# Kernel tuning notes

Hardware: AMD Instinct MI355X
Metric: run time of the kernel (lower is better)

The kernel has to match this reference:

```python
import jax, jax.numpy as jnp
import numpy as np
import math

B, T, C, NH, NLQ, NLKV, DHR = 2, 1024, 2048, 16, 512, 512, 64
HS = C // NH


def _rope(x, cos, sin):
    # x: [B,T,H,D]; cos/sin: [T,D//2]. Rotates pairs (even,odd) like torch apply_rotary_emb.
    xr = x.reshape(x.shape[:-1] + (-1, 2))
    re, im = xr[..., 0], xr[..., 1]
    c = cos[None, :, None, :]
    s = sin[None, :, None, :]
    out = jnp.stack([re * c - im * s, re * s + im * c], axis=-1)
    return out.reshape(x.shape)


def setup_inputs() -> dict:
    key = jax.random.key(0)
    ks = jax.random.split(key, 9)
    sc = jnp.float32(0.02)
    x = jax.random.normal(ks[0], (B, T, C), jnp.float32)
    W_dq = jax.random.normal(ks[1], (NLQ, C), jnp.float32) * sc
    W_uq = jax.random.normal(ks[2], (C, NLQ), jnp.float32) * sc
    W_dkv = jax.random.normal(ks[3], (NLKV, C), jnp.float32) * sc
    W_uk = jax.random.normal(ks[4], (C, NLKV), jnp.float32) * sc
    W_uv = jax.random.normal(ks[5], (C, NLKV), jnp.float32) * sc
    W_qr = jax.random.normal(ks[6], (NH * DHR, NLQ), jnp.float32) * sc
    W_kr = jax.random.normal(ks[7], (DHR, C), jnp.float32) * sc
    W_o = jax.random.normal(ks[8], (C, C), jnp.float32) * sc
    inv = 1.0 / (10000.0 ** (np.arange(0, DHR, 2, dtype=np.float64) / DHR))
    fr = np.outer(np.arange(T), inv)
    freqs_cos = jnp.asarray(np.cos(fr), jnp.float32)
    freqs_sin = jnp.asarray(np.sin(fr), jnp.float32)
    return {"x": x, "freqs_cos": freqs_cos, "freqs_sin": freqs_sin,
            "W_dq": W_dq, "W_uq": W_uq, "W_dkv": W_dkv, "W_uk": W_uk,
            "W_uv": W_uv, "W_qr": W_qr, "W_kr": W_kr, "W_o": W_o}


def reference(x, freqs_cos, freqs_sin, W_dq, W_uq, W_dkv, W_uk, W_uv, W_qr, W_kr, W_o):
    # Training path of FullMHLA (no kv_cache, dropout=0).
    # Absorbed matrices: same memory reinterpretation as torch .view on [out,in] weights.
    k_eff = jnp.einsum('qhd,hdk->hqk', W_uq.reshape(NLQ, NH, HS), W_uk.reshape(NH, HS, NLKV))  # [nh,nlq,nlkv]
    v_eff = (W_uv.T @ W_o.T).reshape(NLKV, NH, HS)  # used as [nlkv,nh,hs]

    c_q = x @ W_dq.T            # [B,T,nlq]
    c_kv = x @ W_dkv.T          # [B,T,nlkv]

    # content scores: c_q @ k_eff @ c_kv^T
    q_abs = jnp.einsum('btq,hqk->bhtk', c_q, k_eff)          # [B,nh,T,nlkv]
    attn_c = jnp.einsum('bhtk,bsk->bhts', q_abs, c_kv)       # [B,nh,T,T]

    # decoupled RoPE scores
    c_kr = x @ W_kr.T                                         # [B,T,dhr]
    k_r = _rope(c_kr[:, :, None, :], freqs_cos, freqs_sin)[:, :, 0, :]   # [B,T,dhr]
    c_qr = (c_q @ W_qr.T).reshape(B, T, NH, DHR)
    q_r = _rope(c_qr, freqs_cos, freqs_sin)                   # [B,T,nh,dhr]
    attn_r = jnp.einsum('bthd,bsd->bhts', q_r, k_r)           # [B,nh,T,T]

    attn = (attn_c + attn_r) / math.sqrt(HS + DHR)
    mask = jnp.triu(jnp.ones((T, T), dtype=bool), k=1)
    attn = jnp.where(mask[None, None], jnp.float32(-jnp.inf), attn)
    attn = jax.nn.softmax(attn, axis=-1)

    # y = attn @ c_kv @ v_eff
    lat = jnp.einsum('bhts,bsk->bhtk', attn, c_kv)            # [B,nh,T,nlkv]
    y = jnp.einsum('bhtk,khd->bthd', lat, v_eff)              # [B,T,nh,hs]
    return y.reshape(B, T, C)
```

## Files before the change

### kernel.cpp

```cpp
#include <hip/hip_runtime.h>

#define Bv   2
#define Tv   1024
#define Cv   2048
#define NHv  16

typedef unsigned short u16;
typedef __attribute__((ext_vector_type(8))) short bf8_t;
typedef __attribute__((ext_vector_type(4))) float f4_t;
typedef __attribute__((ext_vector_type(4))) unsigned short u16x4;
typedef __attribute__((ext_vector_type(8))) unsigned short u16x8;

__device__ __forceinline__ u16 f2bf(float f) {
  union { float f; unsigned u; } v; v.f = f;
  unsigned r = v.u + 0x7fffu + ((v.u >> 16) & 1u);
  return (u16)(r >> 16);
}
__device__ __forceinline__ float bf2f(u16 b) {
  return __uint_as_float((unsigned)b << 16);
}
__device__ __forceinline__ void glds16(const u16* gp, u16* lp) {
  __builtin_amdgcn_global_load_lds(
      (const __attribute__((address_space(1))) void*)gp,
      (__attribute__((address_space(3))) void*)lp, 16, 0, 0);
}

struct Job {
  const u16* A; const u16* B; void* C;
  long sA1, sA2, sB1, sB2, sC1, sC2;
  int K, lda, ldb, ldc, Nact, zdiv, ntx, nty, out_bf;
};
struct JobPack3 { Job j[3]; int cum[4]; };

__global__ __launch_bounds__(256) void gemm_multi(JobPack3 P) {
  const int bid = blockIdx.x;
  const int ji = (bid >= P.cum[1] ? 1 : 0) + (bid >= P.cum[2] ? 1 : 0);
  const Job& J = P.j[ji];
  int local = bid - P.cum[ji];
  const int x = local % J.ntx;
  int rest = local / J.ntx;
  const int y = rest % J.nty;
  const int z = rest / J.nty;
  const int m0 = y * 128, n0 = x * 128;

  const int z1 = z / J.zdiv, z2 = z % J.zdiv;
  const u16* A = J.A + z1 * J.sA1 + z2 * J.sA2;
  const u16* B = J.B + z1 * J.sB1 + z2 * J.sB2;
  const int K = J.K, lda = J.lda, ldb = J.ldb, ldc = J.ldc, Nact = J.Nact;

  __shared__ u16 SMEM[16384];
  u16* As = SMEM;
  u16* Bs = SMEM + 8192;

  const int tid = threadIdx.x, w = tid >> 6, ln = tid & 63;
  const int my = w >> 1, mx = w & 1;
  const int g = ln >> 4, m = ln & 15;

  f4_t acc[4][4];
#pragma unroll
  for (int i = 0; i < 4; ++i)
#pragma unroll
    for (int j = 0; j < 4; ++j) acc[i][j] = (f4_t)0.f;

  for (int k0 = 0; k0 < K; k0 += 64) {
#pragma unroll
    for (int q = 0; q < 4; ++q) {
      int r = 32 * w + 8 * q + (ln >> 3);
      int c = ((ln & 7) - r) & 7;
      glds16(&A[(long)(m0 + r) * lda + k0 + c * 8], &As[(32 * w + 8 * q) * 64]);
      glds16(&B[(long)(n0 + r) * ldb + k0 + c * 8], &Bs[(32 * w + 8 * q) * 64]);
    }
    __syncthreads();
#pragma unroll
    for (int kh = 0; kh < 2; ++kh) {
      bf8_t af[4], bg[4];
#pragma unroll
      for (int mt = 0; mt < 4; ++mt) {
        int row = my * 64 + mt * 16 + m;
        af[mt] = *(const bf8_t*)&As[row * 64 + (((kh * 4 + g) + row) & 7) * 8];
      }
#pragma unroll
      for (int nt = 0; nt < 4; ++nt) {
        int row = mx * 64 + nt * 16 + m;
        bg[nt] = *(const bf8_t*)&Bs[row * 64 + (((kh * 4 + g) + row) & 7) * 8];
      }
#pragma unroll
      for (int mt = 0; mt < 4; ++mt)
#pragma unroll
        for (int nt = 0; nt < 4; ++nt)
          acc[mt][nt] = __builtin_amdgcn_mfma_f32_16x16x32_bf16(
              af[mt], bg[nt], acc[mt][nt], 0, 0, 0);
    }
    __syncthreads();
  }

  if (J.out_bf) {
    u16* Es = SMEM + w * 4096;
#pragma unroll
    for (int mt = 0; mt < 4; ++mt)
#pragma unroll
      for (int nt = 0; nt < 4; ++nt)
#pragma unroll
        for (int r = 0; r < 4; ++r) {
          int row = mt * 16 + g * 4 + r;
          int col = nt * 16 + m;
          Es[row * 64 + (((col >> 3) + row) & 7) * 8 + (col & 7)] =
              f2bf(acc[mt][nt][r]);
        }
    __syncthreads();
    u16* C = (u16*)J.C + z1 * J.sC1 + z2 * J.sC2;
    const long rowbase = (long)(m0 + my * 64 + ln) * ldc + n0 + mx * 64;
#pragma unroll
    for (int c = 0; c < 8; ++c) {
      if (n0 + mx * 64 + c * 8 < Nact) {
        u16x8 v = *(const u16x8*)&Es[ln * 64 + ((c + ln) & 7) * 8];
        *(u16x8*)&C[rowbase + c * 8] = v;
      }
    }
  } else {
    float* C = (float*)J.C + z1 * J.sC1 + z2 * J.sC2;
#pragma unroll
    for (int mt = 0; mt < 4; ++mt)
#pragma unroll
      for (int nt = 0; nt < 4; ++nt)
#pragma unroll
        for (int r = 0; r < 4; ++r) {
          int row = m0 + my * 64 + mt * 16 + g * 4 + r;
          int col = n0 + mx * 64 + nt * 16 + m;
          if (col < Nact) C[(long)row * ldc + col] = acc[mt][nt][r];
        }
  }
}

__global__ __launch_bounds__(256, 3) void attn_part(
    const u16* __restrict__ Qcat,
    const u16* __restrict__ Kcat,
    const u16* __restrict__ ZT,
    float* __restrict__ Opart,
    float* __restrict__ ml,
    float* __restrict__ out) {
  const int x = blockIdx.x;
  const int bh = x & 31, item = x >> 5;
  const int b = bh >> 4, h = bh & 15;
  static const int qtab[40] = {2,3,4,5,6,6,7,7,8,8,9,9,10,10,10,11,11,11,
                               12,12,12,13,13,13,14,14,14,14,15,15,15,15,
                               0,1,4,5,8,9,12,13};
  static const int ctab[40] = {0,0,0,0,0,1,0,1,0,1,0,1,0,1,2,0,1,2,
                               0,1,2,0,1,2,0,1,2,3,0,1,2,3,
                               0,0,1,1,2,2,3,3};
  const int qt = qtab[item], ch = ctab[item];
  const int ns = (qt >> 1) + 1;
  const int s0t = 2 * ch, s1t = min(2 * ch + 2, ns);
  const bool full = (ch == 0) && (qt <= 3);

  __shared__ u16 Bs[8192];
  __shared__ u16 Ps[8192];

  const int tid = threadIdx.x, w = tid >> 6, ln = tid & 63;
  const int g = ln >> 4, m = ln & 15;

  const u16* Qb = Qcat + (long)bh * 589824 + (long)qt * 64 * 576;
  const u16* Kb = Kcat + (long)b * 589824;
  const u16* Zb = ZT + (long)bh * 131072;

  const long qoff = (long)(16 * w + m) * 576;

  f4_t O[8];
#pragma unroll
  for (int j = 0; j < 8; ++j) O[j] = (f4_t)0.f;
  float mrow[4], lrow[4];
#pragma unroll
  for (int r = 0; r < 4; ++r) { mrow[r] = -3e38f; lrow[r] = 0.f; }

  const float scale = 0.07216878364870322f;

  for (int st = s0t; st < s1t; ++st) {
    f4_t S[8];
#pragma unroll
    for (int j = 0; j < 8; ++j) S[j] = (f4_t)0.f;

#pragma unroll 1
    for (int k0 = 0; k0 < 576; k0 += 64) {
#pragma unroll
      for (int q = 0; q < 4; ++q) {
        int r = 32 * w + 8 * q + (ln >> 3);
        int c = ((ln & 7) - r) & 7;
        glds16(&Kb[(long)(st * 128 + r) * 576 + k0 + c * 8],
               &Bs[(32 * w + 8 * q) * 64]);
      }
      bf8_t af0 = *(const bf8_t*)&Qb[qoff + k0 + g * 8];
      bf8_t af1 = *(const bf8_t*)&Qb[qoff + k0 + 32 + g * 8];
      __syncthreads();
#pragma unroll
      for (int kh = 0; kh < 2; ++kh) {
        bf8_t af = kh ? af1 : af0;
#pragma unroll
        for (int nt = 0; nt < 8; ++nt) {
          int row = nt * 16 + m;
          bf8_t bb = *(const bf8_t*)&Bs[row * 64 + (((kh * 4 + g) + row) & 7) * 8];
          S[nt] = __builtin_amdgcn_mfma_f32_16x16x32_bf16(af, bb, S[nt], 0, 0, 0);
        }
      }
      __syncthreads();
    }

    const bool diag = (st == (qt >> 1));
#pragma unroll
    for (int nt = 0; nt < 8; ++nt)
#pragma unroll
      for (int r = 0; r < 4; ++r) {
        float v = S[nt][r] * scale;
        if (diag &&
            (st * 128 + nt * 16 + m) > (qt * 64 + 16 * w + g * 4 + r))
          v = -3e38f;
        S[nt][r] = v;
      }

#pragma unroll
    for (int r = 0; r < 4; ++r) {
      float mx = S[0][r];
#pragma unroll
      for (int nt = 1; nt < 8; ++nt) mx = fmaxf(mx, S[nt][r]);
#pragma unroll
      for (int o = 1; o < 16; o <<= 1) mx = fmaxf(mx, __shfl_xor(mx, o, 64));
      float mn = fmaxf(mrow[r], mx);
      float al = __expf(mrow[r] - mn);
      mrow[r] = mn;
      float rs = 0.f;
#pragma unroll
      for (int nt = 0; nt < 8; ++nt) {
        float p = __expf(S[nt][r] - mn);
        S[nt][r] = p;
        rs += p;
      }
#pragma unroll
      for (int o = 1; o < 16; o <<= 1) rs += __shfl_xor(rs, o, 64);
      lrow[r] = lrow[r] * al + rs;
#pragma unroll
      for (int nt = 0; nt < 8; ++nt) O[nt][r] *= al;
    }

#pragma unroll
    for (int nt = 0; nt < 8; ++nt) {
      int colc = nt * 2 + (m >> 3), cole = m & 7;
#pragma unroll
      for (int r = 0; r < 4; ++r) {
        int row = 16 * w + g * 4 + r;
        Ps[row * 128 + ((colc + row) & 15) * 8 + cole] = f2bf(S[nt][r]);
      }
    }

#pragma unroll
    for (int kb = 0; kb < 2; ++kb) {
      __syncthreads();
#pragma unroll
      for (int q = 0; q < 4; ++q) {
        int r = 32 * w + 8 * q + (ln >> 3);
        int c = ((ln & 7) - r) & 7;
        glds16(&Zb[(long)r * 1024 + st * 128 + kb * 64 + c * 8],
               &Bs[(32 * w + 8 * q) * 64]);
      }
      __syncthreads();
#pragma unroll
      for (int kh = 0; kh < 2; ++kh) {
        int qrow = 16 * w + m;
        int chk = kb * 8 + kh * 4 + g;
        bf8_t af = *(const bf8_t*)&Ps[qrow * 128 + ((chk + qrow) & 15) * 8];
#pragma unroll
        for (int nt = 0; nt < 8; ++nt) {
          int row = nt * 16 + m;
          bf8_t bb = *(const bf8_t*)&Bs[row * 64 + (((kh * 4 + g) + row) & 7) * 8];
          O[nt] = __builtin_amdgcn_mfma_f32_16x16x32_bf16(af, bb, O[nt], 0, 0, 0);
        }
      }
    }
    __syncthreads();
  }

  if (full) {
    float* ob = out + ((long)b * Tv + qt * 64 + 16 * w) * 2048 + h * 128;
#pragma unroll
    for (int r = 0; r < 4; ++r) {
      float inv = 1.0f / lrow[r];
#pragma unroll
      for (int nt = 0; nt < 8; ++nt)
        ob[(long)(g * 4 + r) * 2048 + nt * 16 + m] = O[nt][r] * inv;
    }
  } else {
    float* Ob = Opart + (long)x * 8192;
#pragma unroll
    for (int r = 0; r < 4; ++r) {
      int row = 16 * w + g * 4 + r;
#pragma unroll
      for (int nt = 0; nt < 8; ++nt)
        Ob[(long)row * 128 + nt * 16 + m] = O[nt][r];
      if (m == 0) {
        ml[(long)x * 128 + row] = mrow[r];
        ml[(long)x * 128 + 64 + row] = lrow[r];
      }
    }
  }
}

__global__ __launch_bounds__(256) void attn_merge(
    const float* __restrict__ Opart, const float* __restrict__ ml,
    float* __restrict__ out) {
  const int i = blockIdx.x;
  const int rg = i & 3;
  const int combo = i >> 2;
  const int bh = combo & 31, qt = 4 + (combo >> 5);
  const int b = bh >> 4, h = bh & 15;
  static const int NCH[16] = {1,1,1,1,2,2,2,2,3,3,3,3,4,4,4,4};
  static const int ITEM[64] = {
      32,0,0,0,  33,0,0,0,  0,0,0,0,   1,0,0,0,
      2,34,0,0,  3,35,0,0,  4,5,0,0,   6,7,0,0,
      8,9,36,0,  10,11,37,0, 12,13,14,0, 15,16,17,0,
      18,19,20,38, 21,22,23,39, 24,25,26,27, 28,29,30,31};
  const int nch = NCH[qt];
  const int r = threadIdx.x >> 5, c4 = threadIdx.x & 31;
  float* ob = out + ((long)b * Tv + qt * 64 + rg * 16) * 2048 + h * 128;
#pragma unroll
  for (int rr = 0; rr < 2; ++rr) {
    const int lrow = r + rr * 8;
    const int row = rg * 16 + lrow;
    float M = -3e38f, mi[4], li[4];
    for (int k = 0; k < nch; ++k) {
      long p = (long)ITEM[qt * 4 + k] * 32 + bh;
      mi[k] = ml[p * 128 + row];
      li[k] = ml[p * 128 + 64 + row];
      M = fmaxf(M, mi[k]);
    }
    float L = 0.f;
    float ax = 0.f, ay = 0.f, az = 0.f, aw = 0.f;
    for (int k = 0; k < nch; ++k) {
      long p = (long)ITEM[qt * 4 + k] * 32 + bh;
      float e = __expf(mi[k] - M);
      L += li[k] * e;
      float4 v = *(const float4*)&Opart[p * 8192 + (long)row * 128 + c4 * 4];
      ax += v.x * e; ay += v.y * e; az += v.z * e; aw += v.w * e;
    }
    const float inv = 1.0f / L;
    float4 o4 = {ax * inv, ay * inv, az * inv, aw * inv};
    *(float4*)&ob[(long)lrow * 2048 + c4 * 4] = o4;
  }
}

struct CastArgs {
  const float* src[6];
  u16* dst[6];
  long cum[7];
  const float* wkr;
  u16* w3;
};
__global__ void cast_all(CastArgs a, long total4) {
  long i = (long)blockIdx.x * 256 + threadIdx.x;
  if (i < total4) {
    int seg = 0;
    while (i >= a.cum[seg + 1]) ++seg;
    long j = i - a.cum[seg];
    float4 vv = ((const float4*)a.src[seg])[j];
    u16x4 o;
    o[0] = f2bf(vv.x); o[1] = f2bf(vv.y); o[2] = f2bf(vv.z); o[3] = f2bf(vv.w);
    ((u16x4*)a.dst[seg])[j] = o;
  } else {
    long j = i - total4;
    u16x4* W4 = (u16x4*)a.w3;
    if (j < 32768) {
      float4 vv = ((const float4*)a.wkr)[j];
      u16x4 o;
      o[0] = f2bf(vv.x); o[1] = f2bf(vv.y); o[2] = f2bf(vv.z); o[3] = f2bf(vv.w);
      W4[557056 + j] = o;
    } else if (j < 65536) {
      W4[262144 + (j - 32768)] = (u16x4)0;
    } else {
      W4[589824 + (j - 65536)] = (u16x4)0;
    }
  }
}

__global__ __launch_bounds__(256) void tcast2(const float* __restrict__ s0,
                                              u16* __restrict__ d0,
                                              const float* __restrict__ s1,
                                              u16* __restrict__ d1) {
  const float* in = blockIdx.z ? s1 : s0;
  u16* out = blockIdx.z ? d1 : d0;
  __shared__ u16 t[32][33];
  int c0 = blockIdx.x * 32, r0 = blockIdx.y * 32;
  int tx = threadIdx.x & 31, ty = threadIdx.x >> 5;
  for (int i = ty; i < 32; i += 8)
    t[i][tx] = f2bf(in[(long)(r0 + i) * 512 + c0 + tx]);
  __syncthreads();
  for (int i = ty; i < 32; i += 8)
    out[(long)(c0 + i) * 2048 + r0 + tx] = t[tx][i];
}

__global__ void rope_fused(u16* __restrict__ Kcat, const u16* __restrict__ cqr,
                           u16* __restrict__ Qcat,
                           const float* __restrict__ cosf,
                           const float* __restrict__ sinf) {
  int idx = blockIdx.x * 256 + threadIdx.x;
  if (idx < 65536) {
    int i = idx & 31, t = (idx >> 5) & 1023, b = idx >> 15;
    float c = cosf[t * 32 + i], s = sinf[t * 32 + i];
    u16* p = Kcat + ((long)(b * Tv + t) * 576 + 512 + 2 * i);
    float re = bf2f(p[0]), im = bf2f(p[1]);
    p[0] = f2bf(re * c - im * s);
    p[1] = f2bf(re * s + im * c);
  } else {
    int j = idx - 65536;
    int i = j & 31, h = (j >> 5) & 15, t = (j >> 9) & 1023, b = j >> 19;
    float c = cosf[t * 32 + i], s = sinf[t * 32 + i];
    const u16* src = cqr + ((long)(b * Tv + t) * 1024 + h * 64 + 2 * i);
    float re = bf2f(src[0]), im = bf2f(src[1]);
    u16* dst = Qcat + (((long)(b * NHv + h) * Tv + t) * 576 + 512 + 2 * i);
    dst[0] = f2bf(re * c - im * s);
    dst[1] = f2bf(re * s + im * c);
  }
}

__global__ void vred(const float* __restrict__ P, u16* __restrict__ veffT) {
  int i = blockIdx.x * 256 + threadIdx.x;
  float4 v0 = ((const float4*)P)[i];
  float4 v1 = ((const float4*)P)[262144 + i];
  float4 v2 = ((const float4*)P)[524288 + i];
  float4 v3 = ((const float4*)P)[786432 + i];
  u16x4 o;
  o[0] = f2bf(v0.x + v1.x + v2.x + v3.x);
  o[1] = f2bf(v0.y + v1.y + v2.y + v3.y);
  o[2] = f2bf(v0.z + v1.z + v2.z + v3.z);
  o[3] = f2bf(v0.w + v1.w + v2.w + v3.w);
  ((u16x4*)veffT)[i] = o;
}

extern "C" void kernel_launch(void* const* d_in, const int* in_sizes, int n_in,
                              void* d_out, int out_size, void* d_ws,
                              size_t ws_size, hipStream_t stream) {
  const float* x    = (const float*)d_in[0];
  const float* fcos = (const float*)d_in[1];
  const float* fsin = (const float*)d_in[2];
  const float* Wdq  = (const float*)d_in[3];
  const float* Wuq  = (const float*)d_in[4];
  const float* Wdkv = (const float*)d_in[5];
  const float* Wuk  = (const float*)d_in[6];
  const float* Wuv  = (const float*)d_in[7];
  const float* Wqr  = (const float*)d_in[8];
  const float* Wkr  = (const float*)d_in[9];
  const float* Wo   = (const float*)d_in[10];
  float* out = (float*)d_out;

  u16* ws = (u16*)d_ws;
  u16* cq     = ws;
  u16* Kcat   = cq + 1179648;
  u16* veffT  = Kcat + 1179648;
  u16* Qcat   = veffT + 1048576;
  u16* W3     = Qcat + 18874368;
  u16* x_bf   = W3 + 2490368;
  u16* Wqr_bf = x_bf + 4194304;
  u16* Wuq_bf = Wqr_bf + 524288;
  u16* Wo_bf  = Wuq_bf + 1048576;
  u16* WukT   = Wo_bf + 4194304;
  u16* WuvT   = WukT + 1048576;
  u16* cqr    = WuvT + 1048576;
  u16* keffT  = cqr + 2097152;
  u16* ZTbuf  = keffT + 4194304;
  float* Vprt  = (float*)(ZTbuf + 4194304);
  float* Opart = Vprt + 4194304;
  float* mlbuf = Opart + 10485760;

  {
    CastArgs a;
    a.src[0] = x;    a.dst[0] = x_bf;
    a.src[1] = Wdq;  a.dst[1] = W3;
    a.src[2] = Wdkv; a.dst[2] = W3 + 576 * 2048;
    a.src[3] = Wqr;  a.dst[3] = Wqr_bf;
    a.src[4] = Wuq;  a.dst[4] = Wuq_bf;
    a.src[5] = Wo;   a.dst[5] = Wo_bf;
    a.cum[0] = 0;        a.cum[1] = 1048576; a.cum[2] = 1310720;
    a.cum[3] = 1572864;  a.cum[4] = 1703936; a.cum[5] = 1966080;
    a.cum[6] = 3014656;
    a.wkr = Wkr; a.w3 = W3;
    cast_all<<<12160, 256, 0, stream>>>(a, 3014656L);
  }
  tcast2<<<dim3(16, 64, 2), 256, 0, stream>>>(Wuk, WukT, Wuv, WuvT);

  {
    JobPack3 P;
    P.j[0] = {x_bf, W3, cq, 0, 0, (long)576 * 2048, 0, 1179648, 0,
              2048, 2048, 2048, 576, 576, 1, 5, 16, 1};
    P.j[1] = {Wo_bf, WuvT, Vprt, 512, 0, 512, 0, 1048576, 0,
              512, 2048, 2048, 512, 512, 1, 4, 16, 0};
    P.j[2] = {WukT, Wuq_bf, keffT, 0, 128, 0, 128, 0, 262144,
              128, 2048, 2048, 512, 512, 16, 4, 4, 1};
    P.cum[0] = 0; P.cum[1] = 160; P.cum[2] = 416; P.cum[3] = 672;
    gemm_multi<<<672, 256, 0, stream>>>(P);
  }
  vred<<<1024, 256, 0, stream>>>(Vprt, veffT);

  {
    JobPack3 P;
    P.j[0] = {cq, keffT, Qcat, 589824, 0, 0, 262144, 9437184, 589824,
              512, 576, 512, 576, 512, 16, 4, 8, 1};
    P.j[1] = {veffT, Kcat, ZTbuf, 0, 65536, 589824, 0, 2097152, 131072,
              512, 512, 576, 1024, 1024, 16, 8, 1, 1};
    P.j[2] = {cq, Wqr_bf, cqr, 0, 0, 0, 0, 0, 0,
              512, 576, 512, 1024, 1024, 1, 8, 16, 1};
    P.cum[0] = 0; P.cum[1] = 1024; P.cum[2] = 1280; P.cum[3] = 1408;
    gemm_multi<<<1408, 256, 0, stream>>>(P);
  }

  rope_fused<<<4352, 256, 0, stream>>>(Kcat, cqr, Qcat, fcos, fsin);

  attn_part<<<1280, 256, 0, stream>>>(Qcat, Kcat, ZTbuf, Opart, mlbuf, out);
  attn_merge<<<1536, 256, 0, stream>>>(Opart, mlbuf, out);
}
```

Measured before the change: 289.7 us.

## Use 128-row query tiles with 32x32x16 MFMA in attention kernel

Doubles the query tile from 64 to 128 rows per block and switches from 16x16x32 to 32x32x16 bf16 MFMA. Each wave now owns 32 rows, so every K/Z tile loaded into LDS is reused across twice as many queries. The work tables for split chunks and the merge indexing are rebuilt for the new tile size, and the grid is halved. The cost is more registers (occupancy hint lowered from 3 to 2), a larger P buffer in LDS, fewer blocks to balance across CUs, and more wasted work on the causal diagonal tile.

```diff
diff --git a/kernel.cpp b/kernel.cpp
--- a/kernel.cpp
+++ b/kernel.cpp
@@ -8,6 +8,7 @@
 typedef unsigned short u16;
 typedef __attribute__((ext_vector_type(8))) short bf8_t;
 typedef __attribute__((ext_vector_type(4))) float f4_t;
+typedef __attribute__((ext_vector_type(16))) float f32x16;
 typedef __attribute__((ext_vector_type(4))) unsigned short u16x4;
 typedef __attribute__((ext_vector_type(8))) unsigned short u16x8;
 
@@ -132,7 +133,7 @@
   }
 }
 
-__global__ __launch_bounds__(256, 3) void attn_part(
+__global__ __launch_bounds__(256, 2) void attn_part(
     const u16* __restrict__ Qcat,
     const u16* __restrict__ Kcat,
     const u16* __restrict__ ZT,
@@ -142,42 +143,38 @@
   const int x = blockIdx.x;
   const int bh = x & 31, item = x >> 5;
   const int b = bh >> 4, h = bh & 15;
-  static const int qtab[40] = {2,3,4,5,6,6,7,7,8,8,9,9,10,10,10,11,11,11,
-                               12,12,12,13,13,13,14,14,14,14,15,15,15,15,
-                               0,1,4,5,8,9,12,13};
-  static const int ctab[40] = {0,0,0,0,0,1,0,1,0,1,0,1,0,1,2,0,1,2,
-                               0,1,2,0,1,2,0,1,2,3,0,1,2,3,
-                               0,0,1,1,2,2,3,3};
+  static const int qtab[20] = {1,2,3,3,4,4,5,5,5,6,6,6,7,7,7,7, 0,2,4,6};
+  static const int ctab[20] = {0,0,0,1,0,1,0,1,2,0,1,2,0,1,2,3, 0,1,2,3};
   const int qt = qtab[item], ch = ctab[item];
-  const int ns = (qt >> 1) + 1;
+  const int ns = qt + 1;
   const int s0t = 2 * ch, s1t = min(2 * ch + 2, ns);
-  const bool full = (ch == 0) && (qt <= 3);
+  const bool full = (ch == 0) && (qt <= 1);
 
   __shared__ u16 Bs[8192];
-  __shared__ u16 Ps[8192];
+  __shared__ u16 Ps[16384];
 
   const int tid = threadIdx.x, w = tid >> 6, ln = tid & 63;
-  const int g = ln >> 4, m = ln & 15;
-
-  const u16* Qb = Qcat + (long)bh * 589824 + (long)qt * 64 * 576;
+  const int l5 = ln >> 5, c31 = ln & 31;
+
+  const u16* Qb = Qcat + (long)bh * 589824 + (long)qt * 128 * 576;
   const u16* Kb = Kcat + (long)b * 589824;
   const u16* Zb = ZT + (long)bh * 131072;
 
-  const long qoff = (long)(16 * w + m) * 576;
-
-  f4_t O[8];
-#pragma unroll
-  for (int j = 0; j < 8; ++j) O[j] = (f4_t)0.f;
-  float mrow[4], lrow[4];
-#pragma unroll
-  for (int r = 0; r < 4; ++r) { mrow[r] = -3e38f; lrow[r] = 0.f; }
+  const long qoff = (long)(w * 32 + c31) * 576 + l5 * 8;
+
+  f32x16 O[4];
+#pragma unroll
+  for (int d = 0; d < 4; ++d) O[d] = (f32x16)0.f;
+  float mrow[16], lrow[16];
+#pragma unroll
+  for (int r = 0; r < 16; ++r) { mrow[r] = -3e38f; lrow[r] = 0.f; }
 
   const float scale = 0.07216878364870322f;
 
   for (int st = s0t; st < s1t; ++st) {
-    f4_t S[8];
-#pragma unroll
-    for (int j = 0; j < 8; ++j) S[j] = (f4_t)0.f;
+    f32x16 S[4];
+#pragma unroll
+    for (int a = 0; a < 4; ++a) S[a] = (f32x16)0.f;
 
 #pragma unroll 1
     for (int k0 = 0; k0 < 576; k0 += 64) {
@@ -188,65 +185,66 @@
         glds16(&Kb[(long)(st * 128 + r) * 576 + k0 + c * 8],
                &Bs[(32 * w + 8 * q) * 64]);
       }
-      bf8_t af0 = *(const bf8_t*)&Qb[qoff + k0 + g * 8];
-      bf8_t af1 = *(const bf8_t*)&Qb[qoff + k0 + 32 + g * 8];
+      bf8_t af[4];
+#pragma unroll
+      for (int ks = 0; ks < 4; ++ks)
+        af[ks] = *(const bf8_t*)&Qb[qoff + k0 + ks * 16];
       __syncthreads();
 #pragma unroll
-      for (int kh = 0; kh < 2; ++kh) {
-        bf8_t af = kh ? af1 : af0;
-#pragma unroll
-        for (int nt = 0; nt < 8; ++nt) {
-          int row = nt * 16 + m;
-          bf8_t bb = *(const bf8_t*)&Bs[row * 64 + (((kh * 4 + g) + row) & 7) * 8];
-          S[nt] = __builtin_amdgcn_mfma_f32_16x16x32_bf16(af, bb, S[nt], 0, 0, 0);
+      for (int ks = 0; ks < 4; ++ks) {
+        const int chunk = ks * 2 + l5;
+#pragma unroll
+        for (int a = 0; a < 4; ++a) {
+          int row = a * 32 + c31;
+          bf8_t bb = *(const bf8_t*)&Bs[row * 64 + ((chunk + row) & 7) * 8];
+          S[a] = __builtin_amdgcn_mfma_f32_32x32x16_bf16(af[ks], bb, S[a],
+                                                         0, 0, 0);
         }
       }
       __syncthreads();
     }
 
-    const bool diag = (st == (qt >> 1));
-#pragma unroll
-    for (int nt = 0; nt < 8; ++nt)
-#pragma unroll
-      for (int r = 0; r < 4; ++r) {
-        float v = S[nt][r] * scale;
+    const bool diag = (st == qt);
+#pragma unroll
+    for (int a = 0; a < 4; ++a)
+#pragma unroll
+      for (int r = 0; r < 16; ++r) {
+        float v = S[a][r] * scale;
         if (diag &&
-            (st * 128 + nt * 16 + m) > (qt * 64 + 16 * w + g * 4 + r))
+            (a * 32 + c31) > (w * 32 + (r & 3) + 8 * (r >> 2) + 4 * l5))
           v = -3e38f;
-        S[nt][r] = v;
-      }
-
-#pragma unroll
-    for (int r = 0; r < 4; ++r) {
-      float mx = S[0][r];
-#pragma unroll
-      for (int nt = 1; nt < 8; ++nt) mx = fmaxf(mx, S[nt][r]);
-#pragma unroll
-      for (int o = 1; o < 16; o <<= 1) mx = fmaxf(mx, __shfl_xor(mx, o, 64));
+        S[a][r] = v;
+      }
+
+#pragma unroll
+    for (int r = 0; r < 16; ++r) {
+      float mx = fmaxf(fmaxf(S[0][r], S[1][r]), fmaxf(S[2][r], S[3][r]));
+#pragma unroll
+      for (int o = 1; o < 32; o <<= 1) mx = fmaxf(mx, __shfl_xor(mx, o, 64));
       float mn = fmaxf(mrow[r], mx);
       float al = __expf(mrow[r] - mn);
       mrow[r] = mn;
       float rs = 0.f;
 #pragma unroll
-      for (int nt = 0; nt < 8; ++nt) {
-        float p = __expf(S[nt][r] - mn);
-        S[nt][r] = p;
+      for (int a = 0; a < 4; ++a) {
+        float p = __expf(S[a][r] - mn);
+        S[a][r] = p;
         rs += p;
       }
 #pragma unroll
-      for (int o = 1; o < 16; o <<= 1) rs += __shfl_xor(rs, o, 64);
+      for (int o = 1; o < 32; o <<= 1) rs += __shfl_xor(rs, o, 64);
       lrow[r] = lrow[r] * al + rs;
 #pragma unroll
-      for (int nt = 0; nt < 8; ++nt) O[nt][r] *= al;
-    }
-
-#pragma unroll
-    for (int nt = 0; nt < 8; ++nt) {
-      int colc = nt * 2 + (m >> 3), cole = m & 7;
-#pragma unroll
-      for (int r = 0; r < 4; ++r) {
-        int row = 16 * w + g * 4 + r;
-        Ps[row * 128 + ((colc + row) & 15) * 8 + cole] = f2bf(S[nt][r]);
+      for (int a = 0; a < 4; ++a) O[a][r] *= al;
+    }
+
+#pragma unroll
+    for (int a = 0; a < 4; ++a) {
+      const int colc = a * 4 + (c31 >> 3), cole = c31 & 7;
+#pragma unroll
+      for (int r = 0; r < 16; ++r) {
+        int row = w * 32 + (r & 3) + 8 * (r >> 2) + 4 * l5;
+        Ps[row * 128 + ((colc + row) & 15) * 8 + cole] = f2bf(S[a][r]);
       }
     }
 
@@ -261,16 +259,18 @@
                &Bs[(32 * w + 8 * q) * 64]);
       }
       __syncthreads();
-#pragma unroll
-      for (int kh = 0; kh < 2; ++kh) {
-        int qrow = 16 * w + m;
-        int chk = kb * 8 + kh * 4 + g;
-        bf8_t af = *(const bf8_t*)&Ps[qrow * 128 + ((chk + qrow) & 15) * 8];
-#pragma unroll
-        for (int nt = 0; nt < 8; ++nt) {
-          int row = nt * 16 + m;
-          bf8_t bb = *(const bf8_t*)&Bs[row * 64 + (((kh * 4 + g) + row) & 7) * 8];
-          O[nt] = __builtin_amdgcn_mfma_f32_16x16x32_bf16(af, bb, O[nt], 0, 0, 0);
+      const int prow = w * 32 + c31;
+#pragma unroll
+      for (int ks = 0; ks < 4; ++ks) {
+        const int pchunk = kb * 8 + ks * 2 + l5;
+        bf8_t af = *(const bf8_t*)&Ps[prow * 128 + ((pchunk + prow) & 15) * 8];
+        const int zchunk = ks * 2 + l5;
+#pragma unroll
+        for (int d = 0; d < 4; ++d) {
+          int row = d * 32 + c31;
+          bf8_t bb = *(const bf8_t*)&Bs[row * 64 + ((zchunk + row) & 7) * 8];
+          O[d] = __builtin_amdgcn_mfma_f32_32x32x16_bf16(af, bb, O[d],
+                                                         0, 0, 0);
         }
       }
     }
@@ -278,25 +278,26 @@
   }
 
   if (full) {
-    float* ob = out + ((long)b * Tv + qt * 64 + 16 * w) * 2048 + h * 128;
-#pragma unroll
-    for (int r = 0; r < 4; ++r) {
+    float* ob = out + ((long)b * Tv + qt * 128) * 2048 + h * 128;
+#pragma unroll
+    for (int r = 0; r < 16; ++r) {
       float inv = 1.0f / lrow[r];
-#pragma unroll
-      for (int nt = 0; nt < 8; ++nt)
-        ob[(long)(g * 4 + r) * 2048 + nt * 16 + m] = O[nt][r] * inv;
+      int row = w * 32 + (r & 3) + 8 * (r >> 2) + 4 * l5;
+#pragma unroll
+      for (int d = 0; d < 4; ++d)
+        ob[(long)row * 2048 + d * 32 + c31] = O[d][r] * inv;
     }
   } else {
-    float* Ob = Opart + (long)x * 8192;
-#pragma unroll
-    for (int r = 0; r < 4; ++r) {
-      int row = 16 * w + g * 4 + r;
-#pragma unroll
-      for (int nt = 0; nt < 8; ++nt)
-        Ob[(long)row * 128 + nt * 16 + m] = O[nt][r];
-      if (m == 0) {
-        ml[(long)x * 128 + row] = mrow[r];
-        ml[(long)x * 128 + 64 + row] = lrow[r];
+    float* Ob = Opart + (long)x * 16384;
+#pragma unroll
+    for (int r = 0; r < 16; ++r) {
+      int row = w * 32 + (r & 3) + 8 * (r >> 2) + 4 * l5;
+#pragma unroll
+      for (int d = 0; d < 4; ++d)
+        Ob[row * 128 + d * 32 + c31] = O[d][r];
+      if (c31 == 0) {
+        ml[(long)x * 256 + row] = mrow[r];
+        ml[(long)x * 256 + 128 + row] = lrow[r];
       }
     }
   }
@@ -306,19 +307,18 @@
     const float* __restrict__ Opart, const float* __restrict__ ml,
     float* __restrict__ out) {
   const int i = blockIdx.x;
-  const int rg = i & 3;
-  const int combo = i >> 2;
-  const int bh = combo & 31, qt = 4 + (combo >> 5);
+  const int rg = i & 7;
+  const int combo = i >> 3;
+  const int bh = combo & 31, qt = 2 + (combo >> 5);
   const int b = bh >> 4, h = bh & 15;
-  static const int NCH[16] = {1,1,1,1,2,2,2,2,3,3,3,3,4,4,4,4};
-  static const int ITEM[64] = {
-      32,0,0,0,  33,0,0,0,  0,0,0,0,   1,0,0,0,
-      2,34,0,0,  3,35,0,0,  4,5,0,0,   6,7,0,0,
-      8,9,36,0,  10,11,37,0, 12,13,14,0, 15,16,17,0,
-      18,19,20,38, 21,22,23,39, 24,25,26,27, 28,29,30,31};
+  static const int NCH[8] = {0, 0, 2, 2, 3, 3, 4, 4};
+  static const int ITEM[32] = {
+      0,0,0,0,   0,0,0,0,
+      1,17,0,0,  2,3,0,0,  4,5,18,0,  6,7,8,0,
+      9,10,11,19, 12,13,14,15};
   const int nch = NCH[qt];
   const int r = threadIdx.x >> 5, c4 = threadIdx.x & 31;
-  float* ob = out + ((long)b * Tv + qt * 64 + rg * 16) * 2048 + h * 128;
+  float* ob = out + ((long)b * Tv + qt * 128 + rg * 16) * 2048 + h * 128;
 #pragma unroll
   for (int rr = 0; rr < 2; ++rr) {
     const int lrow = r + rr * 8;
@@ -326,8 +326,8 @@
     float M = -3e38f, mi[4], li[4];
     for (int k = 0; k < nch; ++k) {
       long p = (long)ITEM[qt * 4 + k] * 32 + bh;
-      mi[k] = ml[p * 128 + row];
-      li[k] = ml[p * 128 + 64 + row];
+      mi[k] = ml[p * 256 + row];
+      li[k] = ml[p * 256 + 128 + row];
       M = fmaxf(M, mi[k]);
     }
     float L = 0.f;
@@ -336,7 +336,7 @@
       long p = (long)ITEM[qt * 4 + k] * 32 + bh;
       float e = __expf(mi[k] - M);
       L += li[k] * e;
-      float4 v = *(const float4*)&Opart[p * 8192 + (long)row * 128 + c4 * 4];
+      float4 v = *(const float4*)&Opart[p * 16384 + (long)row * 128 + c4 * 4];
       ax += v.x * e; ay += v.y * e; az += v.z * e; aw += v.w * e;
     }
     const float inv = 1.0f / L;
@@ -510,6 +510,6 @@
 
   rope_fused<<<4352, 256, 0, stream>>>(Kcat, cqr, Qcat, fcos, fsin);
 
-  attn_part<<<1280, 256, 0, stream>>>(Qcat, Kcat, ZTbuf, Opart, mlbuf, out);
+  attn_part<<<640, 256, 0, stream>>>(Qcat, Kcat, ZTbuf, Opart, mlbuf, out);
   attn_merge<<<1536, 256, 0, stream>>>(Opart, mlbuf, out);
 }
```

After: 331.5 us. 14.4% more time.
